# Kernel optimization log

Measured on AMD Instinct MI355X. Metric: run time of the kernel, lower is better.

Reference implementation:

```python
import jax, jax.numpy as jnp
import numpy as np

USER_NUM = 100000
ITEM_NUM = 50000
N_NODES = USER_NUM + ITEM_NUM
EMB = 64
N_LAYERS = 3
N_EDGES = 4000000


def setup_inputs() -> dict:
    key = jax.random.key(0)
    k1, k2, k3, k4, k5 = jax.random.split(key, 5)
    user_emb = jax.random.normal(k1, (USER_NUM, EMB), dtype=jnp.float32)
    item_emb = jax.random.normal(k2, (ITEM_NUM, EMB), dtype=jnp.float32)
    # COO sparse normalized adjacency (values would be 1/sqrt(deg_u*deg_v) in the real graph)
    edge_vals = jax.random.uniform(k3, (N_EDGES,), dtype=jnp.float32)
    edge_src = jax.random.randint(k4, (N_EDGES,), 0, N_NODES, dtype=jnp.int32)
    edge_dst = jax.random.randint(k5, (N_EDGES,), 0, N_NODES, dtype=jnp.int32)
    return {"user_emb": user_emb, "item_emb": item_emb, "edge_vals": edge_vals,
            "edge_src": edge_src, "edge_dst": edge_dst}


def reference(user_emb, item_emb, edge_vals, edge_src, edge_dst):
    # emb = cat([user_emb, item_emb])  -> [N, d]
    emb = jnp.concatenate([user_emb, item_emb], axis=0)
    acc = emb  # running sum over layer embeddings (fuses stack+mean)
    for _ in range(N_LAYERS):
        # SpMM: (A @ emb) via gather -> scale -> segment scatter-add
        msg = edge_vals[:, None] * emb[edge_src]          # [E, d]
        emb = jax.ops.segment_sum(msg, edge_dst, num_segments=N_NODES)
        acc = acc + emb
    final_emb = acc / jnp.float32(N_LAYERS + 1)            # mean over L+1 layer embeddings
    # original returns (final_emb[:user_num], final_emb[user_num:], all_emb);
    # user/item split is a trivial slice of this single array
    return final_emb
```

## Files before the change

### kernel.cpp

```cpp
#include <hip/hip_runtime.h>
#include <hip/hip_fp16.h>

constexpr int USER_NUM = 100000;
constexpr int ITEM_NUM = 50000;
constexpr int N_NODES  = USER_NUM + ITEM_NUM;
constexpr int EMB      = 64;
constexpr int N_LAYERS = 3;
constexpr int NB       = (N_NODES + 255) >> 8;
constexpr int TILE     = 4096;
constexpr int CAP      = 8184;


__device__ inline unsigned pack_f16_2(float a, float b) {
    __half2 h = __floats2half2_rn(a, b);
    return __builtin_bit_cast(unsigned, h);
}

__device__ inline float2 unp_f16_2(unsigned u) {
    return __half22float2(__builtin_bit_cast(__half2, u));
}

__device__ inline void hfma4(uint4 u, __half2 v, __half2* a) {
    a[0] = __hfma2(__builtin_bit_cast(__half2, u.x), v, a[0]);
    a[1] = __hfma2(__builtin_bit_cast(__half2, u.y), v, a[1]);
    a[2] = __hfma2(__builtin_bit_cast(__half2, u.z), v, a[2]);
    a[3] = __hfma2(__builtin_bit_cast(__half2, u.w), v, a[3]);
}


__global__ __launch_bounds__(256) void init_f16_k(const float4* __restrict__ user,
                                                  const float4* __restrict__ item,
                                                  uint4* __restrict__ embA,
                                                  int total8, int user8) {
    int g = blockIdx.x * 256 + threadIdx.x;
    if (g >= total8) return;
    const float4* s4;
    int base;
    if (g < user8) { s4 = user; base = g * 2; }
    else           { s4 = item; base = (g - user8) * 2; }
    float4 lo = s4[base];
    float4 hi = s4[base + 1];
    uint4 o;
    o.x = pack_f16_2(lo.x, lo.y);
    o.y = pack_f16_2(lo.z, lo.w);
    o.z = pack_f16_2(hi.x, hi.y);
    o.w = pack_f16_2(hi.z, hi.w);
    embA[g] = o;
}


__global__ __launch_bounds__(256) void partition_k(const float* __restrict__ vals,
                                                   const int* __restrict__ src,
                                                   const int* __restrict__ dst,
                                                   int* __restrict__ gcursor,
                                                   unsigned* __restrict__ rkey,
                                                   float* __restrict__ rval,
                                                   int n_edges) {
    __shared__ int lhist[NB];
    __shared__ int loff[NB];
    __shared__ int lcur[NB];
    __shared__ int gb[NB];
    __shared__ unsigned stage_k[TILE];
    __shared__ float    stage_v[TILE];
    __shared__ unsigned short stage_b[TILE];

    int tid = threadIdx.x;
    int base = blockIdx.x * TILE;
    int n = min(TILE, n_edges - base);

    for (int b = tid; b < NB; b += 256) lhist[b] = 0;
    __syncthreads();

    for (int k = tid; k < n; k += 256)
        atomicAdd(&lhist[dst[base + k] >> 8], 1);
    __syncthreads();

    if (tid < 64) {
        int carry = 0;
        #pragma unroll
        for (int c = 0; c < (NB + 63) / 64; ++c) {
            int idx = c * 64 + tid;
            int v = (idx < NB) ? lhist[idx] : 0;
            int x = v;
            #pragma unroll
            for (int off = 1; off < 64; off <<= 1) {
                int y = __shfl_up(x, off);
                if (tid >= off) x += y;
            }
            if (idx < NB) { loff[idx] = carry + x - v; lcur[idx] = carry + x - v; }
            carry += __shfl(x, 63);
        }
    }
    __syncthreads();

    for (int k = tid; k < n; k += 256) {
        int e = base + k;
        int d = dst[e];
        int b = d >> 8;
        int slot = atomicAdd(&lcur[b], 1);
        stage_k[slot] = (unsigned)src[e] | ((unsigned)(d & 255) << 18);
        stage_v[slot] = vals[e];
        stage_b[slot] = (unsigned short)b;
    }
    __syncthreads();

    for (int b = tid; b < NB; b += 256) {
        int c = lcur[b] - loff[b];
        if (c > 0) gb[b] = atomicAdd(&gcursor[b], c);
    }
    __syncthreads();

    for (int slot = tid; slot < n; slot += 256) {
        int b = stage_b[slot];
        int rel = gb[b] + (slot - loff[b]);
        if (rel < CAP) {
            size_t pos = (size_t)b * CAP + rel;
            rkey[pos] = stage_k[slot];
            rval[pos] = stage_v[slot];
        }
    }
}

__global__ __launch_bounds__(256) void csrfin_k(const int* __restrict__ gcursor,
                                                const unsigned* __restrict__ rkey,
                                                const float* __restrict__ rval,
                                                unsigned* __restrict__ pairs,
                                                int* __restrict__ rowbeg,
                                                int* __restrict__ rowend) {
    __shared__ int lhist[256];
    __shared__ int lcur[256];
    __shared__ int wsum[4];
    int b = blockIdx.x;
    int node_base = b << 8;
    int nn = min(256, N_NODES - node_base);
    int tid = threadIdx.x;
    int cnt = min(gcursor[b], CAP);
    int rbase = b * CAP;

    lhist[tid] = 0;
    __syncthreads();
    for (int i = tid; i < cnt; i += 256)
        atomicAdd(&lhist[rkey[rbase + i] >> 18], 1);
    __syncthreads();

    int lane = tid & 63, wid = tid >> 6;
    int v = lhist[tid];
    int x = v;
    #pragma unroll
    for (int off = 1; off < 64; off <<= 1) {
        int y = __shfl_up(x, off);
        if (lane >= off) x += y;
    }
    if (lane == 63) wsum[wid] = x;
    __syncthreads();
    if (tid == 0) {
        int c = 0;
        #pragma unroll
        for (int j = 0; j < 4; ++j) { int t = wsum[j]; wsum[j] = c; c += t; }
    }
    __syncthreads();
    int excl = wsum[wid] + x - v;
    if (tid < nn) {
        rowbeg[node_base + tid] = rbase + excl;
        rowend[node_base + tid] = rbase + excl + v;
        lcur[tid] = rbase + excl;
    }
    __syncthreads();

    for (int i = tid; i < cnt; i += 256) {
        unsigned k = rkey[rbase + i];
        float    w = rval[rbase + i];
        int local = (int)(k >> 18);
        unsigned s = k & 0x3FFFFu;
        unsigned valq = min((unsigned)(w * 16384.0f + 0.5f), 16383u);
        int pos = atomicAdd(&lcur[local], 1);
        pairs[pos] = s | (valq << 18);
    }
}


template <int LAST>
__global__ __launch_bounds__(256) void gather_k(const int* __restrict__ rowbeg,
                                                const int* __restrict__ rowend,
                                                const unsigned* __restrict__ pairs,
                                                const uint4* __restrict__ emb,
                                                uint4* __restrict__ nxt,
                                                float4* __restrict__ outf,
                                                const uint4* __restrict__ e1,
                                                const uint4* __restrict__ e2,
                                                const float4* __restrict__ user,
                                                const float4* __restrict__ item) {
    int wid  = threadIdx.x >> 6;
    int node = blockIdx.x * 4 + wid;
    if (node >= N_NODES) return;
    int lane = threadIdx.x & 63;
    int sub  = lane >> 3;
    int q    = lane & 7;

    int beg = rowbeg[node];
    int end = rowend[node];

    __half2 h0[4], h1[4], h2[4], h3[4];
    #pragma unroll
    for (int j = 0; j < 4; ++j) {
        h0[j] = __float2half2_rn(0.0f);
        h1[j] = __float2half2_rn(0.0f);
        h2[j] = __float2half2_rn(0.0f);
        h3[j] = __float2half2_rn(0.0f);
    }

    const float kInv = 1.0f / 16384.0f;
    for (int p = beg; p < end; p += 32) {
        int i0 = p + sub, i1 = p + 8 + sub, i2 = p + 16 + sub, i3 = p + 24 + sub;
        unsigned u0 = (i0 < end) ? pairs[i0] : 0u;
        unsigned u1 = (i1 < end) ? pairs[i1] : 0u;
        unsigned u2 = (i2 < end) ? pairs[i2] : 0u;
        unsigned u3 = (i3 < end) ? pairs[i3] : 0u;
        uint4 x0 = emb[(size_t)(u0 & 0x3FFFFu) * 8 + q];
        uint4 x1 = emb[(size_t)(u1 & 0x3FFFFu) * 8 + q];
        uint4 x2 = emb[(size_t)(u2 & 0x3FFFFu) * 8 + q];
        uint4 x3 = emb[(size_t)(u3 & 0x3FFFFu) * 8 + q];
        hfma4(x0, __float2half2_rn((float)(u0 >> 18) * kInv), h0);
        hfma4(x1, __float2half2_rn((float)(u1 >> 18) * kInv), h1);
        hfma4(x2, __float2half2_rn((float)(u2 >> 18) * kInv), h2);
        hfma4(x3, __float2half2_rn((float)(u3 >> 18) * kInv), h3);
    }

    float s[8];
    #pragma unroll
    for (int j = 0; j < 4; ++j) {
        float2 f0 = __half22float2(h0[j]);
        float2 f1 = __half22float2(h1[j]);
        float2 f2 = __half22float2(h2[j]);
        float2 f3 = __half22float2(h3[j]);
        s[2 * j]     = (f0.x + f1.x) + (f2.x + f3.x);
        s[2 * j + 1] = (f0.y + f1.y) + (f2.y + f3.y);
    }
    #pragma unroll
    for (int j = 0; j < 8; ++j) {
        float t = s[j];
        t += __shfl_xor(t, 8);
        t += __shfl_xor(t, 16);
        t += __shfl_xor(t, 32);
        s[j] = t;
    }

    if (sub == 0) {
        if (LAST) {
            int fb = node * 16 + q * 2;
            float4 u0 = (node < USER_NUM) ? user[fb]     : item[(node - USER_NUM) * 16 + q * 2];
            float4 u1 = (node < USER_NUM) ? user[fb + 1] : item[(node - USER_NUM) * 16 + q * 2 + 1];
            uint4 b1 = e1[(size_t)node * 8 + q];
            uint4 b2 = e2[(size_t)node * 8 + q];
            float2 a1[4], a2[4];
            a1[0] = unp_f16_2(b1.x); a1[1] = unp_f16_2(b1.y);
            a1[2] = unp_f16_2(b1.z); a1[3] = unp_f16_2(b1.w);
            a2[0] = unp_f16_2(b2.x); a2[1] = unp_f16_2(b2.y);
            a2[2] = unp_f16_2(b2.z); a2[3] = unp_f16_2(b2.w);
            float4 r0, r1;
            r0.x = (u0.x + a1[0].x + a2[0].x + s[0]) * 0.25f;
            r0.y = (u0.y + a1[0].y + a2[0].y + s[1]) * 0.25f;
            r0.z = (u0.z + a1[1].x + a2[1].x + s[2]) * 0.25f;
            r0.w = (u0.w + a1[1].y + a2[1].y + s[3]) * 0.25f;
            r1.x = (u1.x + a1[2].x + a2[2].x + s[4]) * 0.25f;
            r1.y = (u1.y + a1[2].y + a2[2].y + s[5]) * 0.25f;
            r1.z = (u1.z + a1[3].x + a2[3].x + s[6]) * 0.25f;
            r1.w = (u1.w + a1[3].y + a2[3].y + s[7]) * 0.25f;
            outf[fb]     = r0;
            outf[fb + 1] = r1;
        } else {
            uint4 o;
            o.x = pack_f16_2(s[0], s[1]);
            o.y = pack_f16_2(s[2], s[3]);
            o.z = pack_f16_2(s[4], s[5]);
            o.w = pack_f16_2(s[6], s[7]);
            nxt[(size_t)node * 8 + q] = o;
        }
    }
}


__global__ __launch_bounds__(256) void fb_init_k(const float4* __restrict__ user,
                                                 const float4* __restrict__ item,
                                                 float4* __restrict__ embA,
                                                 float4* __restrict__ acc,
                                                 int total4, int user4) {
    int i = blockIdx.x * 256 + threadIdx.x;
    if (i >= total4) return;
    float4 v = (i < user4) ? user[i] : item[i - user4];
    embA[i] = v;
    acc[i]  = v;
}

__global__ __launch_bounds__(256) void scatter_k(const float* __restrict__ emb,
                                                 const float* __restrict__ vals,
                                                 const int*   __restrict__ src,
                                                 const int*   __restrict__ dst,
                                                 float* __restrict__ out,
                                                 int n_edges) {
    long long gtid = (long long)blockIdx.x * 256 + threadIdx.x;
    int e = (int)(gtid >> 4);
    if (e >= n_edges) return;
    int lane = (int)(gtid & 15);
    float v = vals[e];
    float4 x = ((const float4*)(emb + (size_t)src[e] * EMB))[lane];
    float* o = out + (size_t)dst[e] * EMB + (size_t)lane * 4;
    unsafeAtomicAdd(o + 0, v * x.x);
    unsafeAtomicAdd(o + 1, v * x.y);
    unsafeAtomicAdd(o + 2, v * x.z);
    unsafeAtomicAdd(o + 3, v * x.w);
}

__global__ __launch_bounds__(256) void acc_k(float4* __restrict__ acc,
                                             const float4* __restrict__ emb, int total4) {
    int i = blockIdx.x * 256 + threadIdx.x;
    if (i >= total4) return;
    float4 a = acc[i], b = emb[i];
    a.x += b.x; a.y += b.y; a.z += b.z; a.w += b.w;
    acc[i] = a;
}

__global__ __launch_bounds__(256) void scale_k(float4* __restrict__ acc, float s, int total4) {
    int i = blockIdx.x * 256 + threadIdx.x;
    if (i >= total4) return;
    float4 a = acc[i];
    a.x *= s; a.y *= s; a.z *= s; a.w *= s;
    acc[i] = a;
}

extern "C" void kernel_launch(void* const* d_in, const int* in_sizes, int n_in,
                              void* d_out, int out_size, void* d_ws, size_t ws_size,
                              hipStream_t stream) {
    const float* user = (const float*)d_in[0];
    const float* item = (const float*)d_in[1];
    const float* vals = (const float*)d_in[2];
    const int*   src  = (const int*)d_in[3];
    const int*   dst  = (const int*)d_in[4];
    float* out = (float*)d_out;

    const int n_edges = in_sizes[2];
    const size_t embf32_bytes = (size_t)N_NODES * EMB * sizeof(float);
    const size_t embf16_bytes = (size_t)N_NODES * EMB * 2;

    const int total4 = N_NODES * EMB / 4;
    const int user4  = USER_NUM * EMB / 4;
    const int total8 = N_NODES * EMB / 8;
    const int user8  = USER_NUM * EMB / 8;
    const int blocks_e4 = (total4 + 255) / 256;
    const int blocks_e8 = (total8 + 255) / 256;

    size_t off = 0;
    uint4*    bufA  = (uint4*)((char*)d_ws + off); off += embf16_bytes;
    uint4*    bufB  = (uint4*)((char*)d_ws + off); off += embf16_bytes;
    uint4*    bufC  = (uint4*)((char*)d_ws + off); off += embf16_bytes;
    unsigned* pairs = (unsigned*)((char*)d_ws + off); off += (size_t)NB * CAP * sizeof(unsigned);
    int*      rowbeg= (int*)((char*)d_ws + off); off += (size_t)N_NODES * sizeof(int);
    int*      rowend= (int*)((char*)d_ws + off); off += (size_t)N_NODES * sizeof(int);
    int*      gcursor=(int*)((char*)d_ws + off); off += (size_t)NB * sizeof(int);

    unsigned* rkey = (unsigned*)bufB;
    float*    rval = (float*)((char*)bufB + (size_t)NB * CAP * sizeof(unsigned));

    if (ws_size < off || n_edges >= (1 << 22)) {
        float* fA = (float*)d_ws;
        float* fB = (float*)((char*)d_ws + embf32_bytes);
        fb_init_k<<<blocks_e4, 256, 0, stream>>>((const float4*)user, (const float4*)item,
                                                 (float4*)fA, (float4*)out, total4, user4);
        const long long work = (long long)n_edges * 16;
        const int blocks_s = (int)((work + 255) / 256);
        float* cur = fA; float* nxt = fB;
        for (int l = 0; l < N_LAYERS; ++l) {
            hipMemsetAsync(nxt, 0, embf32_bytes, stream);
            scatter_k<<<blocks_s, 256, 0, stream>>>(cur, vals, src, dst, nxt, n_edges);
            acc_k<<<blocks_e4, 256, 0, stream>>>((float4*)out, (const float4*)nxt, total4);
            float* t = cur; cur = nxt; nxt = t;
        }
        scale_k<<<blocks_e4, 256, 0, stream>>>((float4*)out, 1.0f / (N_LAYERS + 1), total4);
        return;
    }

    const int blocks_p = (n_edges + TILE - 1) / TILE;
    hipMemsetAsync(gcursor, 0, (size_t)NB * sizeof(int), stream);
    partition_k<<<blocks_p, 256, 0, stream>>>(vals, src, dst, gcursor, rkey, rval, n_edges);
    csrfin_k<<<NB, 256, 0, stream>>>(gcursor, rkey, rval, pairs, rowbeg, rowend);

    init_f16_k<<<blocks_e8, 256, 0, stream>>>((const float4*)user, (const float4*)item,
                                              bufA, total8, user8);

    const int blocks_g = (N_NODES + 3) / 4;
    gather_k<0><<<blocks_g, 256, 0, stream>>>(rowbeg, rowend, pairs, bufA, bufB, nullptr,
                                              nullptr, nullptr, nullptr, nullptr);
    gather_k<0><<<blocks_g, 256, 0, stream>>>(rowbeg, rowend, pairs, bufB, bufC, nullptr,
                                              nullptr, nullptr, nullptr, nullptr);
    gather_k<1><<<blocks_g, 256, 0, stream>>>(rowbeg, rowend, pairs, bufC, nullptr, (float4*)out,
                                              bufB, bufC,
                                              (const float4*)user, (const float4*)item);
}
```

Measured before the change: 331.5 us.

## Drop shared staging in partition, quantize edge values early, widen CSR finalize

The partition kernel no longer histograms, scans and stages edges in shared memory. Each thread keeps 8 edges in registers, takes a per-bucket slot by shared atomic, and writes straight to the global bucket regions, with tile size halved to 2048. Edge values are quantized to 14-bit ushort during partition, so the intermediate buffer carries 2 bytes per value instead of 4. The finalize kernel runs 512 threads per block. Output order inside a bucket becomes nondeterministic and the global writes are less coalesced, but this removes several shared passes and barriers and cuts intermediate traffic.

```diff
diff --git a/kernel.cpp b/kernel.cpp
--- a/kernel.cpp
+++ b/kernel.cpp
@@ -7,7 +7,7 @@
 constexpr int EMB      = 64;
 constexpr int N_LAYERS = 3;
 constexpr int NB       = (N_NODES + 255) >> 8;
-constexpr int TILE     = 4096;
+constexpr int TILE     = 2048;
 constexpr int CAP      = 8184;
 
 
@@ -54,76 +54,57 @@
                                                    const int* __restrict__ dst,
                                                    int* __restrict__ gcursor,
                                                    unsigned* __restrict__ rkey,
-                                                   float* __restrict__ rval,
+                                                   unsigned short* __restrict__ rvalq,
                                                    int n_edges) {
-    __shared__ int lhist[NB];
-    __shared__ int loff[NB];
-    __shared__ int lcur[NB];
+    __shared__ int lcnt[NB];
     __shared__ int gb[NB];
-    __shared__ unsigned stage_k[TILE];
-    __shared__ float    stage_v[TILE];
-    __shared__ unsigned short stage_b[TILE];
-
     int tid = threadIdx.x;
     int base = blockIdx.x * TILE;
     int n = min(TILE, n_edges - base);
 
-    for (int b = tid; b < NB; b += 256) lhist[b] = 0;
-    __syncthreads();
-
-    for (int k = tid; k < n; k += 256)
-        atomicAdd(&lhist[dst[base + k] >> 8], 1);
-    __syncthreads();
-
-    if (tid < 64) {
-        int carry = 0;
-        #pragma unroll
-        for (int c = 0; c < (NB + 63) / 64; ++c) {
-            int idx = c * 64 + tid;
-            int v = (idx < NB) ? lhist[idx] : 0;
-            int x = v;
-            #pragma unroll
-            for (int off = 1; off < 64; off <<= 1) {
-                int y = __shfl_up(x, off);
-                if (tid >= off) x += y;
+    for (int b = tid; b < NB; b += 256) lcnt[b] = 0;
+    __syncthreads();
+
+    unsigned key[8];
+    int rel[8];
+    short bk[8];
+    #pragma unroll
+    for (int j = 0; j < 8; ++j) {
+        int k = j * 256 + tid;
+        if (k < n) {
+            int e = base + k;
+            int d = dst[e];
+            int b = d >> 8;
+            key[j] = (unsigned)src[e] | ((unsigned)(d & 255) << 18);
+            bk[j]  = (short)b;
+            rel[j] = atomicAdd(&lcnt[b], 1);
+        } else bk[j] = -1;
+    }
+    __syncthreads();
+
+    for (int b = tid; b < NB; b += 256) {
+        int c = lcnt[b];
+        if (c > 0) gb[b] = atomicAdd(&gcursor[b], c);
+    }
+    __syncthreads();
+
+    #pragma unroll
+    for (int j = 0; j < 8; ++j) {
+        if (bk[j] >= 0) {
+            int pos = gb[bk[j]] + rel[j];
+            if (pos < CAP) {
+                size_t idx = (size_t)bk[j] * CAP + pos;
+                int e = base + j * 256 + tid;
+                rkey[idx]  = key[j];
+                rvalq[idx] = (unsigned short)min((unsigned)(vals[e] * 16384.0f + 0.5f), 16383u);
             }
-            if (idx < NB) { loff[idx] = carry + x - v; lcur[idx] = carry + x - v; }
-            carry += __shfl(x, 63);
-        }
-    }
-    __syncthreads();
-
-    for (int k = tid; k < n; k += 256) {
-        int e = base + k;
-        int d = dst[e];
-        int b = d >> 8;
-        int slot = atomicAdd(&lcur[b], 1);
-        stage_k[slot] = (unsigned)src[e] | ((unsigned)(d & 255) << 18);
-        stage_v[slot] = vals[e];
-        stage_b[slot] = (unsigned short)b;
-    }
-    __syncthreads();
-
-    for (int b = tid; b < NB; b += 256) {
-        int c = lcur[b] - loff[b];
-        if (c > 0) gb[b] = atomicAdd(&gcursor[b], c);
-    }
-    __syncthreads();
-
-    for (int slot = tid; slot < n; slot += 256) {
-        int b = stage_b[slot];
-        int rel = gb[b] + (slot - loff[b]);
-        if (rel < CAP) {
-            size_t pos = (size_t)b * CAP + rel;
-            rkey[pos] = stage_k[slot];
-            rval[pos] = stage_v[slot];
-        }
-    }
-}
-
-__global__ __launch_bounds__(256) void csrfin_k(const int* __restrict__ gcursor,
+        }
+    }
+}
+
+__global__ __launch_bounds__(512) void csrfin_k(const int* __restrict__ gcursor,
                                                 const unsigned* __restrict__ rkey,
-                                                const float* __restrict__ rval,
+                                                const unsigned short* __restrict__ rvalq,
                                                 unsigned* __restrict__ pairs,
                                                 int* __restrict__ rowbeg,
                                                 int* __restrict__ rowend) {
@@ -137,42 +118,46 @@
     int cnt = min(gcursor[b], CAP);
     int rbase = b * CAP;
 
-    lhist[tid] = 0;
-    __syncthreads();
-    for (int i = tid; i < cnt; i += 256)
+    if (tid < 256) lhist[tid] = 0;
+    __syncthreads();
+    for (int i = tid; i < cnt; i += 512)
         atomicAdd(&lhist[rkey[rbase + i] >> 18], 1);
     __syncthreads();
 
-    int lane = tid & 63, wid = tid >> 6;
-    int v = lhist[tid];
-    int x = v;
-    #pragma unroll
-    for (int off = 1; off < 64; off <<= 1) {
-        int y = __shfl_up(x, off);
-        if (lane >= off) x += y;
-    }
-    if (lane == 63) wsum[wid] = x;
-    __syncthreads();
-    if (tid == 0) {
-        int c = 0;
+    if (tid < 256) {
+        int lane = tid & 63, wid = tid >> 6;
+        int v = lhist[tid];
+        int x = v;
         #pragma unroll
-        for (int j = 0; j < 4; ++j) { int t = wsum[j]; wsum[j] = c; c += t; }
-    }
-    __syncthreads();
-    int excl = wsum[wid] + x - v;
-    if (tid < nn) {
-        rowbeg[node_base + tid] = rbase + excl;
-        rowend[node_base + tid] = rbase + excl + v;
-        lcur[tid] = rbase + excl;
-    }
-    __syncthreads();
-
-    for (int i = tid; i < cnt; i += 256) {
+        for (int off = 1; off < 64; off <<= 1) {
+            int y = __shfl_up(x, off);
+            if (lane >= off) x += y;
+        }
+        if (lane == 63) wsum[wid] = x;
+        __syncthreads();
+        if (tid == 0) {
+            int c = 0;
+            #pragma unroll
+            for (int j = 0; j < 4; ++j) { int t = wsum[j]; wsum[j] = c; c += t; }
+        }
+        __syncthreads();
+        int excl = wsum[wid] + x - v;
+        if (tid < nn) {
+            rowbeg[node_base + tid] = rbase + excl;
+            rowend[node_base + tid] = rbase + excl + v;
+            lcur[tid] = rbase + excl;
+        }
+    } else {
+        __syncthreads();
+        __syncthreads();
+    }
+    __syncthreads();
+
+    for (int i = tid; i < cnt; i += 512) {
         unsigned k = rkey[rbase + i];
-        float    w = rval[rbase + i];
+        unsigned valq = rvalq[rbase + i];
         int local = (int)(k >> 18);
         unsigned s = k & 0x3FFFFu;
-        unsigned valq = min((unsigned)(w * 16384.0f + 0.5f), 16383u);
         int pos = atomicAdd(&lcur[local], 1);
         pairs[pos] = s | (valq << 18);
     }
@@ -358,8 +343,8 @@
     int*      rowend= (int*)((char*)d_ws + off); off += (size_t)N_NODES * sizeof(int);
     int*      gcursor=(int*)((char*)d_ws + off); off += (size_t)NB * sizeof(int);
 
-    unsigned* rkey = (unsigned*)bufB;
-    float*    rval = (float*)((char*)bufB + (size_t)NB * CAP * sizeof(unsigned));
+    unsigned*       rkey  = (unsigned*)bufB;
+    unsigned short* rvalq = (unsigned short*)bufC;
 
     if (ws_size < off || n_edges >= (1 << 22)) {
         float* fA = (float*)d_ws;
@@ -381,8 +366,8 @@
 
     const int blocks_p = (n_edges + TILE - 1) / TILE;
     hipMemsetAsync(gcursor, 0, (size_t)NB * sizeof(int), stream);
-    partition_k<<<blocks_p, 256, 0, stream>>>(vals, src, dst, gcursor, rkey, rval, n_edges);
-    csrfin_k<<<NB, 256, 0, stream>>>(gcursor, rkey, rval, pairs, rowbeg, rowend);
+    partition_k<<<blocks_p, 256, 0, stream>>>(vals, src, dst, gcursor, rkey, rvalq, n_edges);
+    csrfin_k<<<NB, 512, 0, stream>>>(gcursor, rkey, rvalq, pairs, rowbeg, rowend);
 
     init_f16_k<<<blocks_e8, 256, 0, stream>>>((const float4*)user, (const float4*)item,
                                               bufA, total8, user8);
```

New measurement: 400.7 us. +20.9%, slower.
